# Kernel tuning notes

Hardware: AMD Instinct MI355X
Metric: run time of the kernel (lower is better)

## Reference

```python
import jax, jax.numpy as jnp
import numpy as np

WS = 7          # window_size
NH = 8          # num_heads
EMB = 128       # embedding_dim
HD = EMB // NH  # head_dim
SCALE = HD ** -0.5
LN_EPS = 1e-5


def setup_inputs() -> dict:
    key = jax.random.key(0)
    ks = jax.random.split(key, 5)
    B, N, C = 64, 3136, EMB  # H = W = 56
    x = jax.random.normal(ks[0], (B, N, C), dtype=jnp.float32)
    ln_gamma = jnp.ones((C,), dtype=jnp.float32)
    ln_beta = jnp.zeros((C,), dtype=jnp.float32)
    w_qkv = jax.random.normal(ks[1], (C, 3 * C), dtype=jnp.float32) * (C ** -0.5)
    b_qkv = jax.random.normal(ks[2], (3 * C,), dtype=jnp.float32) * 0.02
    w_out = jax.random.normal(ks[3], (C, C), dtype=jnp.float32) * (C ** -0.5)
    b_out = jax.random.normal(ks[4], (C,), dtype=jnp.float32) * 0.02
    return {"x": x, "ln_gamma": ln_gamma, "ln_beta": ln_beta,
            "w_qkv": w_qkv, "b_qkv": b_qkv, "w_out": w_out, "b_out": b_out}


def reference(x, ln_gamma, ln_beta, w_qkv, b_qkv, w_out, b_out):
    B, N, C = x.shape
    H = int(np.sqrt(N))  # static
    Wd = H

    # LayerNorm over last dim
    mu = jnp.mean(x, axis=-1, keepdims=True)
    var = jnp.mean(jnp.square(x - mu), axis=-1, keepdims=True)
    xn = (x - mu) * jax.lax.rsqrt(var + LN_EPS) * ln_gamma + ln_beta

    # divide windows: [B,N,C] -> [B*nWh*nWw, WS*WS, C]
    nW = H // WS
    win = xn.reshape(B, nW, WS, nW, WS, C).transpose(0, 1, 3, 2, 4, 5)
    win = win.reshape(-1, WS * WS, C)

    # QKV projection
    qkv = win @ w_qkv + b_qkv                      # [nw, 49, 3C]
    qkv = qkv.reshape(-1, WS * WS, 3, NH, HD).transpose(2, 0, 3, 1, 4)
    q, k, v = qkv[0], qkv[1], qkv[2]               # [nw, NH, 49, HD]

    scores = jnp.einsum('whqd,whkd->whqk', q, k) * SCALE
    probs = jax.nn.softmax(scores, axis=-1)
    attn = jnp.einsum('whqk,whkd->whqd', probs, v) # [nw, NH, 49, HD]
    attn = attn.transpose(0, 2, 1, 3).reshape(-1, WS * WS, C)

    out = attn @ w_out + b_out                     # [nw, 49, C]

    # merge windows -> [B, H, W, C]
    out = out.reshape(B, nW, nW, WS, WS, C).transpose(0, 1, 3, 2, 4, 5)
    return out.reshape(B, H, Wd, C)
```

## Files before the change

kernel.cpp:

```cpp
#include <hip/hip_runtime.h>

typedef float floatx4 __attribute__((ext_vector_type(4)));
typedef __bf16 bf16t;
typedef __bf16 bf16x8 __attribute__((ext_vector_type(8)));
typedef __bf16 bf16x4 __attribute__((ext_vector_type(4)));
typedef unsigned short u16t;
typedef unsigned int u32t;

static __device__ __forceinline__ u16t f2bf(float f) {
  return __builtin_bit_cast(u16t, (__bf16)f);
}
static __device__ __forceinline__ float bf2f(u16t h) {
  return __uint_as_float((u32t)h << 16);
}

#define MFMA(A, B, C) __builtin_amdgcn_mfma_f32_16x16x32_bf16((A), (B), (C), 0, 0, 0)

__global__ void pack_weights_kernel(const float* __restrict__ wqkv,
                                    const float* __restrict__ wout,
                                    u16t* __restrict__ wq_p,
                                    u16t* __restrict__ wo_p) {
  int g = blockIdx.x * blockDim.x + threadIdx.x;
  int l = g & 63;
  int s = (g >> 6) & 3;
  int n = g >> 8;
  int cl = l & 15;
  if (n < 24) {
    int kbase = 32 * s + ((l >> 4) * 8);
    int col = 16 * n + cl;
    u16t* dst = wq_p + g * 8;
#pragma unroll
    for (int j = 0; j < 8; ++j) dst[j] = f2bf(wqkv[(kbase + j) * 384 + col]);
  } else {
    int col = 16 * (n - 24) + cl;
    u16t* dst = wo_p + (g - 24 * 256) * 8;
    int rbase = 32 * s + 4 * (l >> 4);
#pragma unroll
    for (int j = 0; j < 8; ++j)
      dst[j] = f2bf(wout[(rbase + 16 * (j >> 2) + (j & 3)) * 128 + col]);
  }
}

__global__ __launch_bounds__(256, 4) void win_attn_kernel(
    const float* __restrict__ x, const float* __restrict__ gamma,
    const float* __restrict__ beta, const u16t* __restrict__ wq_p,
    const float* __restrict__ bqkv, const u16t* __restrict__ wo_p,
    const float* __restrict__ bout, float* __restrict__ out) {
  __shared__ u16t xnK[64][136];
  __shared__ u16t xv[9216];

  const int tid = threadIdx.x;
  const int lane = tid & 63;
  const int w = tid >> 6;
  const int llo = lane & 15;
  const int lhi = lane >> 4;

  const int wi = blockIdx.x;
  const int bimg = wi >> 6;
  const int widx = wi & 63;
  const int nwh = widx >> 3;
  const int nww = widx & 7;
  const int base_off = (((bimg * 56) + nwh * 7) * 56 + nww * 7) * 128;
  const float* xbase = x + base_off;

  for (int i = tid; i < 15 * 64; i += 256) {
    int r = 49 + (i >> 6), c = (i & 63) << 1;
    *(u32t*)&xnK[r][c] = 0;
    *(u32t*)&xv[r * 136 + c] = 0;
  }

  {
    const float g0 = gamma[2 * lane], g1 = gamma[2 * lane + 1];
    const float b0 = beta[2 * lane], b1 = beta[2 * lane + 1];
    for (int t = w; t < 49; t += 4) {
      int wr = t / 7, wc = t - wr * 7;
      const float* row = xbase + (wr * 56 + wc) * 128;
      float2 v = *(const float2*)(row + 2 * lane);
      float sm = v.x + v.y;
      float sq = v.x * v.x + v.y * v.y;
#pragma unroll
      for (int m = 1; m < 64; m <<= 1) {
        sm += __shfl_xor(sm, m);
        sq += __shfl_xor(sq, m);
      }
      float mean = sm * (1.f / 128.f);
      float var = sq * (1.f / 128.f) - mean * mean;
      float rs = rsqrtf(var + 1e-5f);
      float y0 = (v.x - mean) * rs * g0 + b0;
      float y1 = (v.y - mean) * rs * g1 + b1;
      u16t h0 = f2bf(y0), h1 = f2bf(y1);
      u16t l0 = f2bf(y0 - bf2f(h0)), l1 = f2bf(y1 - bf2f(h1));
      *(u32t*)&xnK[t][2 * lane] = (u32t)h0 | ((u32t)h1 << 16);
      *(u32t*)&xv[t * 136 + 2 * lane] = (u32t)l0 | ((u32t)l1 << 16);
    }
  }
  __syncthreads();

  const int rowA = 16 * w + llo;
  const int rowC = 16 * w + lhi * 4;
  const floatx4 z4 = {0.f, 0.f, 0.f, 0.f};

  bf16x8 a_hi[4], a_lo[4];
#pragma unroll
  for (int s = 0; s < 4; ++s) {
    a_hi[s] = *(const bf16x8*)&xnK[rowA][s * 32 + lhi * 8];
    a_lo[s] = *(const bf16x8*)&xv[rowA * 136 + s * 32 + lhi * 8];
  }
  bf16x8 bqw[4];
#pragma unroll
  for (int s = 0; s < 4; ++s)
    bqw[s] = *(const bf16x8*)(wq_p + (s * 64 + lane) * 8);
  __syncthreads();

#pragma unroll 2
  for (int h = 0; h < 8; ++h) {
    const u16t* pwk = wq_p + (((8 + h) * 4) * 64 + lane) * 8;
    const u16t* pwv = wq_p + (((16 + h) * 4) * 64 + lane) * 8;
    floatx4 ak = z4, av = z4;
#pragma unroll
    for (int s = 0; s < 4; ++s) {
      bf16x8 bk = *(const bf16x8*)(pwk + s * 512);
      bf16x8 bv = *(const bf16x8*)(pwv + s * 512);
      ak = MFMA(bk, a_hi[s], ak);
      ak = MFMA(bk, a_lo[s], ak);
      av = MFMA(a_hi[s], bv, av);
      av = MFMA(a_lo[s], bv, av);
    }
    float4 bk4 = *(const float4*)(bqkv + 128 + h * 16 + 4 * lhi);
    ushort4 kk;
    kk.x = f2bf(ak[0] + bk4.x);
    kk.y = f2bf(ak[1] + bk4.y);
    kk.z = f2bf(ak[2] + bk4.z);
    kk.w = f2bf(ak[3] + bk4.w);
    *(ushort4*)&xnK[16 * w + llo][h * 16 + 4 * lhi] = kk;
    float bv_ = bqkv[256 + h * 16 + llo];
    ushort4 vv;
    vv.x = f2bf(av[0] + bv_);
    vv.y = f2bf(av[1] + bv_);
    vv.z = f2bf(av[2] + bv_);
    vv.w = f2bf(av[3] + bv_);
    *(ushort4*)&xv[(h * 16 + llo) * 72 + rowC] = vv;
  }

  bf16x8 qf;
  {
    floatx4 aq = z4;
#pragma unroll
    for (int s = 0; s < 4; ++s) aq = MFMA(bqw[s], a_hi[s], aq);
    float4 bq4 = *(const float4*)(bqkv + 4 * lhi);
    float q0 = aq[0] + bq4.x, q1 = aq[1] + bq4.y;
    float q2 = aq[2] + bq4.z, q3 = aq[3] + bq4.w;
    qf[0] = (bf16t)q0; qf[1] = (bf16t)q1;
    qf[2] = (bf16t)q2; qf[3] = (bf16t)q3;
    qf[4] = (bf16t)(q0 - (float)qf[0]);
    qf[5] = (bf16t)(q1 - (float)qf[1]);
    qf[6] = (bf16t)(q2 - (float)qf[2]);
    qf[7] = (bf16t)(q3 - (float)qf[3]);
  }
  __syncthreads();

  bf16x4 kv4[4];
  bf16x4 v00, v01, v10, v11;
  {
#pragma unroll
    for (int n = 0; n < 4; ++n)
      kv4[n] = *(const bf16x4*)&xnK[16 * n + llo][4 * lhi];
    const int vrow = llo * 72;
    v00 = *(const bf16x4*)&xv[vrow + 4 * lhi];
    v01 = *(const bf16x4*)&xv[vrow + 16 + 4 * lhi];
    v10 = *(const bf16x4*)&xv[vrow + 32 + 4 * lhi];
    v11 = *(const bf16x4*)&xv[vrow + 48 + 4 * lhi];
  }

  const float SEXP = 0.25f * 1.44269504088896340736f;
  floatx4 oc[8];
#pragma unroll
  for (int n = 0; n < 8; ++n) oc[n] = z4;

#pragma unroll 1
  for (int p4 = 0; p4 < 4; ++p4) {
    bf16x8 atf;
#pragma unroll
    for (int hp = 0; hp < 2; ++hp) {
      const int h = 2 * p4 + hp;
      if (h < 7) {
        const u16t* pq = wq_p + (((h + 1) * 4) * 64 + lane) * 8;
#pragma unroll
        for (int s = 0; s < 4; ++s) bqw[s] = *(const bf16x8*)(pq + s * 512);
      }

      floatx4 sc[4];
#pragma unroll
      for (int n = 0; n < 4; ++n) {
        bf16x8 kbf =
            __builtin_shufflevector(kv4[n], kv4[n], 0, 1, 2, 3, 0, 1, 2, 3);
        sc[n] = MFMA(kbf, qf, z4);
      }

      bf16x4 nk[4], nv0, nv1, nv2, nv3;
      if (h < 7) {
        const int kcol = (h + 1) * 16 + 4 * lhi;
#pragma unroll
        for (int n = 0; n < 4; ++n)
          nk[n] = *(const bf16x4*)&xnK[16 * n + llo][kcol];
        const int vrow = ((h + 1) * 16 + llo) * 72;
        nv0 = *(const bf16x4*)&xv[vrow + 4 * lhi];
        nv1 = *(const bf16x4*)&xv[vrow + 16 + 4 * lhi];
        nv2 = *(const bf16x4*)&xv[vrow + 32 + 4 * lhi];
        nv3 = *(const bf16x4*)&xv[vrow + 48 + 4 * lhi];
      }

      float s0 = 0.f;
#pragma unroll
      for (int n = 0; n < 4; ++n) {
#pragma unroll
        for (int j = 0; j < 4; ++j) {
          float pe;
          if (n == 3)
            pe = (4 * lhi + j < 1) ? exp2f(sc[n][j] * SEXP) : 0.f;
          else
            pe = exp2f(sc[n][j] * SEXP);
          sc[n][j] = pe;
          s0 += pe;
        }
      }
      s0 += __shfl_xor(s0, 16);
      s0 += __shfl_xor(s0, 32);
      float rq = 1.f / s0;

      bf16x8 PB0, PB1;
#pragma unroll
      for (int j = 0; j < 4; ++j) {
        PB0[j] = (bf16t)sc[0][j];
        PB0[4 + j] = (bf16t)sc[1][j];
        PB1[j] = (bf16t)sc[2][j];
        PB1[4 + j] = (bf16t)sc[3][j];
      }
      bf16x8 V0 = __builtin_shufflevector(v00, v01, 0, 1, 2, 3, 4, 5, 6, 7);
      bf16x8 V1 = __builtin_shufflevector(v10, v11, 0, 1, 2, 3, 4, 5, 6, 7);
      floatx4 ao = MFMA(V0, PB0, z4);
      ao = MFMA(V1, PB1, ao);
      atf[4 * hp + 0] = (bf16t)(ao[0] * rq);
      atf[4 * hp + 1] = (bf16t)(ao[1] * rq);
      atf[4 * hp + 2] = (bf16t)(ao[2] * rq);
      atf[4 * hp + 3] = (bf16t)(ao[3] * rq);

      if (h < 7) {
        floatx4 aq = z4;
#pragma unroll
        for (int s = 0; s < 4; ++s) aq = MFMA(bqw[s], a_hi[s], aq);
        float4 bq4 = *(const float4*)(bqkv + (h + 1) * 16 + 4 * lhi);
        float q0 = aq[0] + bq4.x, q1 = aq[1] + bq4.y;
        float q2 = aq[2] + bq4.z, q3 = aq[3] + bq4.w;
        qf[0] = (bf16t)q0; qf[1] = (bf16t)q1;
        qf[2] = (bf16t)q2; qf[3] = (bf16t)q3;
        qf[4] = (bf16t)(q0 - (float)qf[0]);
        qf[5] = (bf16t)(q1 - (float)qf[1]);
        qf[6] = (bf16t)(q2 - (float)qf[2]);
        qf[7] = (bf16t)(q3 - (float)qf[3]);
#pragma unroll
        for (int n = 0; n < 4; ++n) kv4[n] = nk[n];
        v00 = nv0; v01 = nv1; v10 = nv2; v11 = nv3;
      }
    }
#pragma unroll
    for (int n = 0; n < 8; ++n)
      oc[n] = MFMA(atf,
                   *(const bf16x8*)(wo_p + ((n * 4 + p4) * 64 + lane) * 8),
                   oc[n]);
  }

  float bo[8];
#pragma unroll
  for (int n = 0; n < 8; ++n) bo[n] = bout[16 * n + llo];
  float* obase = out + base_off;
#pragma unroll
  for (int r = 0; r < 4; ++r) {
    int t = rowC + r;
    if (t < 49) {
      int wr = t / 7, wc = t - wr * 7;
      float* orow = obase + (wr * 56 + wc) * 128;
#pragma unroll
      for (int n = 0; n < 8; ++n) orow[16 * n + llo] = oc[n][r] + bo[n];
    }
  }
}

extern "C" void kernel_launch(void* const* d_in, const int* in_sizes, int n_in,
                              void* d_out, int out_size, void* d_ws,
                              size_t ws_size, hipStream_t stream) {
  const float* x = (const float*)d_in[0];
  const float* ln_g = (const float*)d_in[1];
  const float* ln_b = (const float*)d_in[2];
  const float* w_qkv = (const float*)d_in[3];
  const float* b_qkv = (const float*)d_in[4];
  const float* w_out = (const float*)d_in[5];
  const float* b_out = (const float*)d_in[6];
  float* out = (float*)d_out;

  u16t* wq_p = (u16t*)d_ws;
  u16t* wo_p = wq_p + 24 * 256 * 8;

  hipLaunchKernelGGL(pack_weights_kernel, dim3(32), dim3(256), 0, stream,
                     w_qkv, w_out, wq_p, wo_p);
  hipLaunchKernelGGL(win_attn_kernel, dim3(4096), dim3(256), 0, stream, x,
                     ln_g, ln_b, wq_p, b_qkv, wo_p, b_out, out);
}
```

Measured before the change: 331.7 us.

## Precompute all Q heads upfront and fully unroll the attention head loop

Computes Q for all eight heads in one batch before the attention loop and keeps them in registers, instead of computing each next head's Q inside the loop. The head loop is then fully unrolled, and the output projection runs on every second head. The launch attribute moves to amdgpu_waves_per_eu(4,4). The aim is to drop the serialized per-head Q MFMA chain and loop overhead so the compiler can schedule more freely, at the cost of about 32 more VGPRs for qall, which risks spills under the occupancy cap.

Measured after the change: 314.1 us. -5.3%, faster.

```diff
diff --git a/kernel.cpp b/kernel.cpp
--- a/kernel.cpp
+++ b/kernel.cpp
@@ -41,7 +41,8 @@
   }
 }
 
-__global__ __launch_bounds__(256, 4) void win_attn_kernel(
+__global__ __launch_bounds__(256)
+__attribute__((amdgpu_waves_per_eu(4, 4))) void win_attn_kernel(
     const float* __restrict__ x, const float* __restrict__ gamma,
     const float* __restrict__ beta, const u16t* __restrict__ wq_p,
     const float* __restrict__ bqkv, const u16t* __restrict__ wo_p,
@@ -106,10 +107,6 @@
     a_hi[s] = *(const bf16x8*)&xnK[rowA][s * 32 + lhi * 8];
     a_lo[s] = *(const bf16x8*)&xv[rowA * 136 + s * 32 + lhi * 8];
   }
-  bf16x8 bqw[4];
-#pragma unroll
-  for (int s = 0; s < 4; ++s)
-    bqw[s] = *(const bf16x8*)(wq_p + (s * 64 + lane) * 8);
   __syncthreads();
 
 #pragma unroll 2
@@ -142,132 +139,109 @@
     *(ushort4*)&xv[(h * 16 + llo) * 72 + rowC] = vv;
   }
 
-  bf16x8 qf;
-  {
+  bf16x8 qall[8];
+#pragma unroll
+  for (int h = 0; h < 8; ++h) {
+    const u16t* pq = wq_p + ((h * 4) * 64 + lane) * 8;
     floatx4 aq = z4;
 #pragma unroll
-    for (int s = 0; s < 4; ++s) aq = MFMA(bqw[s], a_hi[s], aq);
-    float4 bq4 = *(const float4*)(bqkv + 4 * lhi);
+    for (int s = 0; s < 4; ++s)
+      aq = MFMA(*(const bf16x8*)(pq + s * 512), a_hi[s], aq);
+    float4 bq4 = *(const float4*)(bqkv + h * 16 + 4 * lhi);
     float q0 = aq[0] + bq4.x, q1 = aq[1] + bq4.y;
     float q2 = aq[2] + bq4.z, q3 = aq[3] + bq4.w;
-    qf[0] = (bf16t)q0; qf[1] = (bf16t)q1;
-    qf[2] = (bf16t)q2; qf[3] = (bf16t)q3;
-    qf[4] = (bf16t)(q0 - (float)qf[0]);
-    qf[5] = (bf16t)(q1 - (float)qf[1]);
-    qf[6] = (bf16t)(q2 - (float)qf[2]);
-    qf[7] = (bf16t)(q3 - (float)qf[3]);
+    qall[h][0] = (bf16t)q0;
+    qall[h][1] = (bf16t)q1;
+    qall[h][2] = (bf16t)q2;
+    qall[h][3] = (bf16t)q3;
+    qall[h][4] = (bf16t)(q0 - (float)qall[h][0]);
+    qall[h][5] = (bf16t)(q1 - (float)qall[h][1]);
+    qall[h][6] = (bf16t)(q2 - (float)qall[h][2]);
+    qall[h][7] = (bf16t)(q3 - (float)qall[h][3]);
   }
   __syncthreads();
 
-  bf16x4 kv4[4];
-  bf16x4 v00, v01, v10, v11;
+  bf16x4 kv4[4], vv4[4];
+#pragma unroll
+  for (int n = 0; n < 4; ++n)
+    kv4[n] = *(const bf16x4*)&xnK[16 * n + llo][4 * lhi];
   {
-#pragma unroll
-    for (int n = 0; n < 4; ++n)
-      kv4[n] = *(const bf16x4*)&xnK[16 * n + llo][4 * lhi];
     const int vrow = llo * 72;
-    v00 = *(const bf16x4*)&xv[vrow + 4 * lhi];
-    v01 = *(const bf16x4*)&xv[vrow + 16 + 4 * lhi];
-    v10 = *(const bf16x4*)&xv[vrow + 32 + 4 * lhi];
-    v11 = *(const bf16x4*)&xv[vrow + 48 + 4 * lhi];
+#pragma unroll
+    for (int i = 0; i < 4; ++i)
+      vv4[i] = *(const bf16x4*)&xv[vrow + 16 * i + 4 * lhi];
   }
 
   const float SEXP = 0.25f * 1.44269504088896340736f;
   floatx4 oc[8];
 #pragma unroll
   for (int n = 0; n < 8; ++n) oc[n] = z4;
-
-#pragma unroll 1
-  for (int p4 = 0; p4 < 4; ++p4) {
-    bf16x8 atf;
-#pragma unroll
-    for (int hp = 0; hp < 2; ++hp) {
-      const int h = 2 * p4 + hp;
-      if (h < 7) {
-        const u16t* pq = wq_p + (((h + 1) * 4) * 64 + lane) * 8;
-#pragma unroll
-        for (int s = 0; s < 4; ++s) bqw[s] = *(const bf16x8*)(pq + s * 512);
+  bf16x8 atf;
+
+#pragma unroll
+  for (int h = 0; h < 8; ++h) {
+    floatx4 sc[4];
+#pragma unroll
+    for (int n = 0; n < 4; ++n) {
+      bf16x8 kbf =
+          __builtin_shufflevector(kv4[n], kv4[n], 0, 1, 2, 3, 0, 1, 2, 3);
+      sc[n] = MFMA(kbf, qall[h], z4);
+    }
+    bf16x8 V0 = __builtin_shufflevector(vv4[0], vv4[1], 0, 1, 2, 3, 4, 5, 6, 7);
+    bf16x8 V1 = __builtin_shufflevector(vv4[2], vv4[3], 0, 1, 2, 3, 4, 5, 6, 7);
+    if (h < 7) {
+      const int kcol = (h + 1) * 16 + 4 * lhi;
+#pragma unroll
+      for (int n = 0; n < 4; ++n)
+        kv4[n] = *(const bf16x4*)&xnK[16 * n + llo][kcol];
+      const int vrow = ((h + 1) * 16 + llo) * 72;
+#pragma unroll
+      for (int i = 0; i < 4; ++i)
+        vv4[i] = *(const bf16x4*)&xv[vrow + 16 * i + 4 * lhi];
+    }
+
+    float s0 = 0.f;
+#pragma unroll
+    for (int n = 0; n < 4; ++n) {
+#pragma unroll
+      for (int j = 0; j < 4; ++j) {
+        float pe;
+        if (n == 3)
+          pe = (4 * lhi + j < 1) ? exp2f(sc[n][j] * SEXP) : 0.f;
+        else
+          pe = exp2f(sc[n][j] * SEXP);
+        sc[n][j] = pe;
+        s0 += pe;
       }
-
-      floatx4 sc[4];
-#pragma unroll
-      for (int n = 0; n < 4; ++n) {
-        bf16x8 kbf =
-            __builtin_shufflevector(kv4[n], kv4[n], 0, 1, 2, 3, 0, 1, 2, 3);
-        sc[n] = MFMA(kbf, qf, z4);
-      }
-
-      bf16x4 nk[4], nv0, nv1, nv2, nv3;
-      if (h < 7) {
-        const int kcol = (h + 1) * 16 + 4 * lhi;
-#pragma unroll
-        for (int n = 0; n < 4; ++n)
-          nk[n] = *(const bf16x4*)&xnK[16 * n + llo][kcol];
-        const int vrow = ((h + 1) * 16 + llo) * 72;
-        nv0 = *(const bf16x4*)&xv[vrow + 4 * lhi];
-        nv1 = *(const bf16x4*)&xv[vrow + 16 + 4 * lhi];
-        nv2 = *(const bf16x4*)&xv[vrow + 32 + 4 * lhi];
-        nv3 = *(const bf16x4*)&xv[vrow + 48 + 4 * lhi];
-      }
-
-      float s0 = 0.f;
-#pragma unroll
-      for (int n = 0; n < 4; ++n) {
-#pragma unroll
-        for (int j = 0; j < 4; ++j) {
-          float pe;
-          if (n == 3)
-            pe = (4 * lhi + j < 1) ? exp2f(sc[n][j] * SEXP) : 0.f;
-          else
-            pe = exp2f(sc[n][j] * SEXP);
-          sc[n][j] = pe;
-          s0 += pe;
-        }
-      }
-      s0 += __shfl_xor(s0, 16);
-      s0 += __shfl_xor(s0, 32);
-      float rq = 1.f / s0;
-
-      bf16x8 PB0, PB1;
-#pragma unroll
-      for (int j = 0; j < 4; ++j) {
-        PB0[j] = (bf16t)sc[0][j];
-        PB0[4 + j] = (bf16t)sc[1][j];
-        PB1[j] = (bf16t)sc[2][j];
-        PB1[4 + j] = (bf16t)sc[3][j];
-      }
-      bf16x8 V0 = __builtin_shufflevector(v00, v01, 0, 1, 2, 3, 4, 5, 6, 7);
-      bf16x8 V1 = __builtin_shufflevector(v10, v11, 0, 1, 2, 3, 4, 5, 6, 7);
-      floatx4 ao = MFMA(V0, PB0, z4);
-      ao = MFMA(V1, PB1, ao);
-      atf[4 * hp + 0] = (bf16t)(ao[0] * rq);
-      atf[4 * hp + 1] = (bf16t)(ao[1] * rq);
-      atf[4 * hp + 2] = (bf16t)(ao[2] * rq);
-      atf[4 * hp + 3] = (bf16t)(ao[3] * rq);
-
-      if (h < 7) {
-        floatx4 aq = z4;
-#pragma unroll
-        for (int s = 0; s < 4; ++s) aq = MFMA(bqw[s], a_hi[s], aq);
-        float4 bq4 = *(const float4*)(bqkv + (h + 1) * 16 + 4 * lhi);
-        float q0 = aq[0] + bq4.x, q1 = aq[1] + bq4.y;
-        float q2 = aq[2] + bq4.z, q3 = aq[3] + bq4.w;
-        qf[0] = (bf16t)q0; qf[1] = (bf16t)q1;
-        qf[2] = (bf16t)q2; qf[3] = (bf16t)q3;
-        qf[4] = (bf16t)(q0 - (float)qf[0]);
-        qf[5] = (bf16t)(q1 - (float)qf[1]);
-        qf[6] = (bf16t)(q2 - (float)qf[2]);
-        qf[7] = (bf16t)(q3 - (float)qf[3]);
-#pragma unroll
-        for (int n = 0; n < 4; ++n) kv4[n] = nk[n];
-        v00 = nv0; v01 = nv1; v10 = nv2; v11 = nv3;
-      }
-    }
-#pragma unroll
-    for (int n = 0; n < 8; ++n)
-      oc[n] = MFMA(atf,
-                   *(const bf16x8*)(wo_p + ((n * 4 + p4) * 64 + lane) * 8),
-                   oc[n]);
+    }
+    s0 += __shfl_xor(s0, 16);
+    s0 += __shfl_xor(s0, 32);
+    float rq = 1.f / s0;
+
+    bf16x8 PB0, PB1;
+#pragma unroll
+    for (int j = 0; j < 4; ++j) {
+      PB0[j] = (bf16t)sc[0][j];
+      PB0[4 + j] = (bf16t)sc[1][j];
+      PB1[j] = (bf16t)sc[2][j];
+      PB1[4 + j] = (bf16t)sc[3][j];
+    }
+    floatx4 ao = MFMA(V0, PB0, z4);
+    ao = MFMA(V1, PB1, ao);
+    const int hp = h & 1;
+    atf[4 * hp + 0] = (bf16t)(ao[0] * rq);
+    atf[4 * hp + 1] = (bf16t)(ao[1] * rq);
+    atf[4 * hp + 2] = (bf16t)(ao[2] * rq);
+    atf[4 * hp + 3] = (bf16t)(ao[3] * rq);
+
+    if (hp) {
+      const int p4 = h >> 1;
+#pragma unroll
+      for (int n = 0; n < 8; ++n)
+        oc[n] = MFMA(atf,
+                     *(const bf16x8*)(wo_p + ((n * 4 + p4) * 64 + lane) * 8),
+                     oc[n]);
+    }
   }
 
   float bo[8];
```
